# Performance work log

Measured on AMD Instinct MI355X. Metric: run time of the kernel, lower is better.

## Reference

```python
import jax, jax.numpy as jnp
import numpy as np

B, L, D, H = 2, 384, 256, 8
DH = D // H


def setup_inputs() -> dict:
    key = jax.random.key(0)
    ks = jax.random.split(key, 16)
    xav = lambda k, shape: jax.random.normal(k, shape, jnp.float32) * np.sqrt(2.0 / sum(shape[-2:]))
    return {
        "key": jax.random.normal(ks[0], (B, L, D), jnp.float32),
        "query": jax.random.normal(ks[1], (B, L, D), jnp.float32),
        "value": jax.random.normal(ks[2], (B, L, D), jnp.float32),
        "pos": jax.random.normal(ks[3], (B, L, L, D), jnp.float32),
        "key_mask": jnp.ones((B, L), jnp.float32),
        "Wk": xav(ks[4], (D, D)), "bk": jnp.zeros((D,), jnp.float32),
        "Wq": xav(ks[5], (D, D)), "bq": jnp.zeros((D,), jnp.float32),
        "Wv": xav(ks[6], (D, D)), "bv": jnp.zeros((D,), jnp.float32),
        "Wr": xav(ks[7], (D, D)), "br": jnp.zeros((D,), jnp.float32),
        "u": xav(ks[8], (H, DH)),
        "v": xav(ks[9], (H, DH)),
    }


def reference(key, query, value, pos, key_mask, Wk, bk, Wq, bq, Wv, bv, Wr, br, u, v):
    b, l, d = key.shape
    dh = d // H
    # projections (torch Linear: x @ W.T + b)
    k = (key @ Wk.T + bk).reshape(b, l, H, dh).transpose(0, 2, 1, 3)    # [b,h,l,dh]
    q = (query @ Wq.T + bq).reshape(b, l, H, dh).transpose(0, 2, 1, 3)  # [b,h,l,dh]
    val = (value @ Wv.T + bv).reshape(b, l, H, dh).transpose(0, 2, 1, 3)
    r = (pos @ Wr.T + br).reshape(b, l, l, H, dh)                       # [b,q,k,h,dh]
    # content term A+C: (q + u) @ k^T
    A_C = jnp.einsum("bhqd,bhkd->bhqk", q + u[None, :, None, :], k)
    # position term B+D: (q + v) contracted with per-(q,k) relative embedding
    B_D = jnp.einsum("bhqd,bqkhd->bhqk", q + v[None, :, None, :], r)
    score = (A_C + B_D) / np.sqrt(dh).astype(np.float32)
    score = score - (1.0 - key_mask[:, None, None, :]) * 1e15
    attn = jax.nn.softmax(score, axis=-1)  # dropout is identity at eval
    out = jnp.einsum("bhqk,bhkd->bhqd", attn, val)
    return out.transpose(0, 2, 1, 3).reshape(b, l, d)
```

## Files before the change

### kernel.cpp

```cpp
#include <hip/hip_runtime.h>
#include <math.h>

#define BB 2
#define LL 384
#define DD 256
#define HH 8
#define DHH 32

static const size_t OFF_Q     = 0;
static const size_t OFF_KK    = 196608;
static const size_t OFF_VV    = 393216;
static const size_t OFF_W     = 589824;
static const size_t OFF_CBR   = 2162688;

__device__ __forceinline__ float dot4(float4 a, float4 b) {
    return a.x * b.x + a.y * b.y + a.z * b.z + a.w * b.w;
}

__global__ __launch_bounds__(256) void k_proj(
    const float* __restrict__ Xq, const float* __restrict__ Xk, const float* __restrict__ Xv,
    const float* __restrict__ Wq, const float* __restrict__ Wk, const float* __restrict__ Wv,
    const float* __restrict__ bq, const float* __restrict__ bk, const float* __restrict__ bv,
    float* __restrict__ oq, float* __restrict__ okk, float* __restrict__ ovv)
{
    int bx = blockIdx.x;
    int mat = bx / 96;
    int rem = bx % 96;
    int b = rem / 48;
    int l0 = (rem % 48) * 8;
    const float* X = (mat == 0) ? Xq : (mat == 1) ? Xk : Xv;
    const float* W = (mat == 0) ? Wq : (mat == 1) ? Wk : Wv;
    const float* bias = (mat == 0) ? bq : (mat == 1) ? bk : bv;

    __shared__ float xs[8 * 256];
    int tid = threadIdx.x;
    {
        const float4* src = (const float4*)(X + (size_t)(b * LL + l0) * DD);
        float4* dst = (float4*)xs;
        dst[tid] = src[tid];
        dst[tid + 256] = src[tid + 256];
    }
    __syncthreads();

    int n = tid;
    float bn = bias[n];
    float acc[8];
#pragma unroll
    for (int l = 0; l < 8; ++l) acc[l] = bn;

    const float4* wrow = (const float4*)(W + (size_t)n * DD);
#pragma unroll 8
    for (int kc = 0; kc < 64; ++kc) {
        float4 wv = wrow[kc];
#pragma unroll
        for (int l = 0; l < 8; ++l) {
            float4 xv = ((const float4*)(xs + l * 256))[kc];
            acc[l] += dot4(wv, xv);
        }
    }

    if (mat <= 1) {
        float* o = (mat == 0) ? oq : okk;
#pragma unroll
        for (int l = 0; l < 8; ++l)
            o[(size_t)(b * LL + l0 + l) * DD + n] = acc[l];
    } else {
        int h = n >> 5, dh = n & 31;
#pragma unroll
        for (int l = 0; l < 8; ++l)
            ovv[((size_t)(b * HH + h) * LL + l0 + l) * DHH + dh] = acc[l];
    }
}

__global__ __launch_bounds__(256) void k_wproj(
    const float* __restrict__ q, const float* __restrict__ vpar,
    const float* __restrict__ Wr, const float* __restrict__ br,
    float* __restrict__ w, float* __restrict__ cbr)
{
    int bx = blockIdx.x;
    int b = bx / 384;
    int rem = bx % 384;
    int l0 = (rem >> 2) * 4;
    int hg = rem & 3;
    int tid = threadIdx.x;
    int gq = tid >> 6;
    int lane = tid & 63;

    __shared__ float qv[4][64];
    if (lane < 16) {
        const float* qsrc = q + (size_t)(b * LL + l0 + gq) * DD + hg * 64;
        const float* vsrc = vpar + hg * 64;
        float4 t = *(const float4*)(qsrc + lane * 4);
        float4 vv4 = *(const float4*)(vsrc + lane * 4);
        t.x += vv4.x; t.y += vv4.y; t.z += vv4.z; t.w += vv4.w;
        *(float4*)(&qv[gq][lane * 4]) = t;
    }
    __syncthreads();

    int l = l0 + gq;
    int d4 = lane * 4;
    float* wbase = w + ((size_t)(b * LL + l) * HH) * DD + d4;
#pragma unroll
    for (int h2 = 0; h2 < 2; ++h2) {
        int h = hg * 2 + h2;
        float4 acc = make_float4(0.f, 0.f, 0.f, 0.f);
#pragma unroll 8
        for (int dh = 0; dh < 32; ++dh) {
            float s = qv[gq][h2 * 32 + dh];
            float4 wr4 = *(const float4*)(Wr + (size_t)(h * 32 + dh) * DD + d4);
            acc.x += s * wr4.x; acc.y += s * wr4.y; acc.z += s * wr4.z; acc.w += s * wr4.w;
        }
        *(float4*)(wbase + h * DD) = acc;
    }

    if (tid < 8) {
        int rr = tid >> 1, h2 = tid & 1;
        float s = 0.f;
#pragma unroll 8
        for (int dh = 0; dh < 32; ++dh)
            s += qv[rr][h2 * 32 + dh] * br[hg * 64 + h2 * 32 + dh];
        cbr[(size_t)(b * LL + l0 + rr) * HH + hg * 2 + h2] = s;
    }
}

__global__ __launch_bounds__(256, 2) void k_bdsoft(
    const float* __restrict__ pos, const float* __restrict__ w,
    const float* __restrict__ q, const float* __restrict__ u,
    const float* __restrict__ kk, const float* __restrict__ cbr,
    const float* __restrict__ mask, const float* __restrict__ vv,
    float* __restrict__ out)
{
    int b = blockIdx.x / LL;
    int qi = blockIdx.x % LL;
    int tid = threadIdx.x;
    int wave = tid >> 6;
    int lane = tid & 63;
    int g = lane & 15;
    int r = lane >> 4;

    __shared__ float sld[8][388];

    const float* wb = w + ((size_t)(b * LL + qi) * HH) * DD + g * 4;
    float4 wr[8][4];
#pragma unroll
    for (int h = 0; h < 8; ++h) {
#pragma unroll
        for (int j = 0; j < 4; ++j)
            wr[h][j] = *(const float4*)(wb + h * DD + j * 64);
    }

    float2 qu[8];
    const float* qrow = q + (size_t)(b * LL + qi) * DD + 2 * g;
#pragma unroll
    for (int h = 0; h < 8; ++h) {
        float2 qa = *(const float2*)(qrow + h * 32);
        float2 ua = *(const float2*)(u + h * 32 + 2 * g);
        qu[h] = make_float2(qa.x + ua.x, qa.y + ua.y);
    }
    float cb[8];
#pragma unroll
    for (int h = 0; h < 8; ++h) cb[h] = cbr[(size_t)(b * LL + qi) * HH + h];

    const float* posq = pos + (size_t)(b * LL + qi) * LL * DD + g * 4;
    const float* kkb = kk + (size_t)b * LL * DD + 2 * g;
    const float inv = 0.17677669529663687f;

#pragma unroll 1
    for (int k0 = wave * 4; k0 < LL; k0 += 16) {
        int krow = k0 + r;
        const float* pr = posq + (size_t)krow * DD;
        float4 p0 = *(const float4*)(pr);
        float4 p1 = *(const float4*)(pr + 64);
        float4 p2 = *(const float4*)(pr + 128);
        float4 p3 = *(const float4*)(pr + 192);
        const float* kr = kkb + (size_t)krow * DD;
        float acc[8];
#pragma unroll
        for (int h = 0; h < 8; ++h) {
            float2 kv = *(const float2*)(kr + h * 32);
            acc[h] = dot4(p0, wr[h][0]) + dot4(p1, wr[h][1]) +
                     dot4(p2, wr[h][2]) + dot4(p3, wr[h][3]) +
                     qu[h].x * kv.x + qu[h].y * kv.y;
        }
#pragma unroll
        for (int m = 1; m <= 8; m <<= 1) {
#pragma unroll
            for (int h = 0; h < 8; ++h)
                acc[h] += __shfl_xor(acc[h], m, 64);
        }
        if (g == 0) {
            float pen = (1.0f - mask[b * LL + krow]) * 1e15f;
#pragma unroll
            for (int h = 0; h < 8; ++h)
                sld[h][krow] = (acc[h] + cb[h]) * inv - pen;
        }
    }
    __syncthreads();

#pragma unroll
    for (int hi = 0; hi < 2; ++hi) {
        int h = wave * 2 + hi;
        float s[6];
#pragma unroll
        for (int j = 0; j < 6; ++j) s[j] = sld[h][lane + 64 * j];
        float m = s[0];
#pragma unroll
        for (int j = 1; j < 6; ++j) m = fmaxf(m, s[j]);
#pragma unroll
        for (int off = 1; off < 64; off <<= 1) m = fmaxf(m, __shfl_xor(m, off, 64));
        float e[6];
        float ls = 0.f;
#pragma unroll
        for (int j = 0; j < 6; ++j) { e[j] = __expf(s[j] - m); ls += e[j]; }
#pragma unroll
        for (int off = 1; off < 64; off <<= 1) ls += __shfl_xor(ls, off, 64);
        float rinv = 1.0f / ls;
#pragma unroll
        for (int j = 0; j < 6; ++j) sld[h][lane + 64 * j] = e[j] * rinv;
    }
    __syncthreads();

    int h = tid >> 5, dh = tid & 31;
    const float* vp = vv + ((size_t)(b * HH + h) * LL) * DHH + dh;
    float acc = 0.f;
#pragma unroll 8
    for (int k = 0; k < LL; ++k) {
        acc += sld[h][k] * vp[(size_t)k * DHH];
    }
    out[(size_t)(b * LL + qi) * DD + tid] = acc;
}

extern "C" void kernel_launch(void* const* d_in, const int* in_sizes, int n_in,
                              void* d_out, int out_size, void* d_ws, size_t ws_size,
                              hipStream_t stream) {
    const float* key    = (const float*)d_in[0];
    const float* query  = (const float*)d_in[1];
    const float* value  = (const float*)d_in[2];
    const float* pos    = (const float*)d_in[3];
    const float* kmask  = (const float*)d_in[4];
    const float* Wk     = (const float*)d_in[5];
    const float* bk     = (const float*)d_in[6];
    const float* Wq     = (const float*)d_in[7];
    const float* bq     = (const float*)d_in[8];
    const float* Wv     = (const float*)d_in[9];
    const float* bv     = (const float*)d_in[10];
    const float* Wr     = (const float*)d_in[11];
    const float* br     = (const float*)d_in[12];
    const float* u      = (const float*)d_in[13];
    const float* v      = (const float*)d_in[14];
    float* out = (float*)d_out;

    float* ws = (float*)d_ws;
    float* qbuf   = ws + OFF_Q;
    float* kkbuf  = ws + OFF_KK;
    float* vvbuf  = ws + OFF_VV;
    float* wbuf   = ws + OFF_W;
    float* cbrbuf = ws + OFF_CBR;

    k_proj<<<dim3(288), dim3(256), 0, stream>>>(query, key, value, Wq, Wk, Wv,
                                                bq, bk, bv, qbuf, kkbuf, vvbuf);
    k_wproj<<<dim3(768), dim3(256), 0, stream>>>(qbuf, v, Wr, br, wbuf, cbrbuf);
    k_bdsoft<<<dim3(768), dim3(256), 0, stream>>>(pos, wbuf, qbuf, u, kkbuf,
                                                  cbrbuf, kmask, vvbuf, out);
}
```

Measured before the change: 502.9 us.

## Split content scores into separate pass and use transpose-reduce shuffles in position loop

Moves the q+u·k content term out of the pos-streaming loop into a dedicated pass that writes the masked, scaled score to shared memory. The pos loop now uses 32-lane groups, each handling 8 floats per row, and reduces the eight head sums with a recursive-halving butterfly. This needs fewer shuffles and fewer W registers. It also raises the launch-bounds occupancy hint from 2 to 3 blocks. The aim is to cut register pressure and shuffle count in the bandwidth-bound pos stream, at the cost of an extra shared-memory pass and a read-modify-write on the score array.

```diff
diff --git a/kernel.cpp b/kernel.cpp
--- a/kernel.cpp
+++ b/kernel.cpp
@@ -123,7 +123,7 @@
     }
 }
 
-__global__ __launch_bounds__(256, 2) void k_bdsoft(
+__global__ __launch_bounds__(256, 3) void k_bdsoft(
     const float* __restrict__ pos, const float* __restrict__ w,
     const float* __restrict__ q, const float* __restrict__ u,
     const float* __restrict__ kk, const float* __restrict__ cbr,
@@ -135,65 +135,86 @@
     int tid = threadIdx.x;
     int wave = tid >> 6;
     int lane = tid & 63;
-    int g = lane & 15;
-    int r = lane >> 4;
-
-    __shared__ float sld[8][388];
+    int g = lane & 31;
+    int r = lane >> 5;
+
+    __shared__ float sld[8][390];
+    __shared__ float qs[256];
+
+    const float inv = 0.17677669529663687f;
+
+    qs[tid] = q[(size_t)(b * LL + qi) * DD + tid] + u[tid];
 
     const float* wb = w + ((size_t)(b * LL + qi) * HH) * DD + g * 4;
-    float4 wr[8][4];
+    float4 wr[8][2];
 #pragma unroll
     for (int h = 0; h < 8; ++h) {
-#pragma unroll
-        for (int j = 0; j < 4; ++j)
-            wr[h][j] = *(const float4*)(wb + h * DD + j * 64);
-    }
-
-    float2 qu[8];
-    const float* qrow = q + (size_t)(b * LL + qi) * DD + 2 * g;
-#pragma unroll
-    for (int h = 0; h < 8; ++h) {
-        float2 qa = *(const float2*)(qrow + h * 32);
-        float2 ua = *(const float2*)(u + h * 32 + 2 * g);
-        qu[h] = make_float2(qa.x + ua.x, qa.y + ua.y);
-    }
-    float cb[8];
-#pragma unroll
-    for (int h = 0; h < 8; ++h) cb[h] = cbr[(size_t)(b * LL + qi) * HH + h];
+        wr[h][0] = *(const float4*)(wb + h * DD);
+        wr[h][1] = *(const float4*)(wb + h * DD + 128);
+    }
+    __syncthreads();
+
+    {
+        const float* cbp = cbr + (size_t)(b * LL + qi) * HH;
+#pragma unroll
+        for (int j = 0; j < 12; ++j) {
+            int idx = tid + j * 256;
+            int h = idx / 384;
+            int k = idx - h * 384;
+            const float4* kp = (const float4*)(kk + (size_t)(b * LL + k) * DD + h * 32);
+            const float4* qp = (const float4*)(qs + h * 32);
+            float acc = 0.f;
+#pragma unroll
+            for (int jj = 0; jj < 8; ++jj) acc += dot4(kp[jj], qp[jj]);
+            float pen = (1.0f - mask[b * LL + k]) * 1e15f;
+            sld[h][k] = (acc + cbp[h]) * inv - pen;
+        }
+    }
+    __syncthreads();
 
     const float* posq = pos + (size_t)(b * LL + qi) * LL * DD + g * 4;
-    const float* kkb = kk + (size_t)b * LL * DD + 2 * g;
-    const float inv = 0.17677669529663687f;
+    const float* pr = posq + (size_t)(wave * 2 + r) * DD;
+    int krow = wave * 2 + r;
+    bool b4 = (g & 16) != 0;
+    bool b3 = (g & 8) != 0;
+    bool b2 = (g & 4) != 0;
+    int hown = g >> 2;
+    bool leader = (g & 3) == 0;
 
 #pragma unroll 1
-    for (int k0 = wave * 4; k0 < LL; k0 += 16) {
-        int krow = k0 + r;
-        const float* pr = posq + (size_t)krow * DD;
+    for (int it = 0; it < 48; ++it) {
         float4 p0 = *(const float4*)(pr);
-        float4 p1 = *(const float4*)(pr + 64);
-        float4 p2 = *(const float4*)(pr + 128);
-        float4 p3 = *(const float4*)(pr + 192);
-        const float* kr = kkb + (size_t)krow * DD;
+        float4 p1 = *(const float4*)(pr + 128);
         float acc[8];
 #pragma unroll
-        for (int h = 0; h < 8; ++h) {
-            float2 kv = *(const float2*)(kr + h * 32);
-            acc[h] = dot4(p0, wr[h][0]) + dot4(p1, wr[h][1]) +
-                     dot4(p2, wr[h][2]) + dot4(p3, wr[h][3]) +
-                     qu[h].x * kv.x + qu[h].y * kv.y;
-        }
-#pragma unroll
-        for (int m = 1; m <= 8; m <<= 1) {
-#pragma unroll
-            for (int h = 0; h < 8; ++h)
-                acc[h] += __shfl_xor(acc[h], m, 64);
-        }
-        if (g == 0) {
-            float pen = (1.0f - mask[b * LL + krow]) * 1e15f;
-#pragma unroll
-            for (int h = 0; h < 8; ++h)
-                sld[h][krow] = (acc[h] + cb[h]) * inv - pen;
-        }
+        for (int h = 0; h < 8; ++h)
+            acc[h] = dot4(p0, wr[h][0]) + dot4(p1, wr[h][1]);
+
+        float t0[4];
+#pragma unroll
+        for (int i = 0; i < 4; ++i) {
+            float sendv = b4 ? acc[i] : acc[i + 4];
+            float keepv = b4 ? acc[i + 4] : acc[i];
+            t0[i] = keepv + __shfl_xor(sendv, 16, 64);
+        }
+        float t1[2];
+#pragma unroll
+        for (int i = 0; i < 2; ++i) {
+            float sendv = b3 ? t0[i] : t0[i + 2];
+            float keepv = b3 ? t0[i + 2] : t0[i];
+            t1[i] = keepv + __shfl_xor(sendv, 8, 64);
+        }
+        float sendv = b2 ? t1[0] : t1[1];
+        float keepv = b2 ? t1[1] : t1[0];
+        float vsum = keepv + __shfl_xor(sendv, 4, 64);
+        vsum += __shfl_xor(vsum, 2, 64);
+        vsum += __shfl_xor(vsum, 1, 64);
+
+        if (leader)
+            sld[hown][krow] += vsum * inv;
+
+        pr += 8 * DD;
+        krow += 8;
     }
     __syncthreads();
 
```

Result: no change. 503.7 us (+0.2%).
